# Optimization experiments

Measured on AMD Instinct MI355X. Metric: run time of the kernel, lower is better.

The kernel has to match this reference:

```python
import jax, jax.numpy as jnp
import numpy as np
from jax import lax

N_HEADS = 16
EPS = 1e-6
CHUNK = 128  # chunk size for the causal kv cumsum scan


def causal_dot_product(q, k, v):
    """Equivalent to cumsum over outer-products: out[l] = q[l] . sum_{j<=l} k[j] v[j]^T.
    Chunked lax.scan avoids materializing the [B,H,L,D,M] tensor.
    q,k: [B,H,L,D], v: [B,H,L,M] -> [B,H,L,M]."""
    B, H, L, D = q.shape
    M = v.shape[-1]
    nc = L // CHUNK
    qc = q.reshape(B, H, nc, CHUNK, D).transpose(2, 0, 1, 3, 4)
    kc = k.reshape(B, H, nc, CHUNK, D).transpose(2, 0, 1, 3, 4)
    vc = v.reshape(B, H, nc, CHUNK, M).transpose(2, 0, 1, 3, 4)

    def step(kv_carry, inp):
        qb, kb, vb = inp  # [B,H,C,D], [B,H,C,D], [B,H,C,M]
        kv = jnp.einsum('bhcd,bhcm->bhcdm', kb, vb)
        kv_cum = jnp.cumsum(kv, axis=2) + kv_carry[:, :, None]
        out = jnp.einsum('bhcd,bhcdm->bhcm', qb, kv_cum)
        return kv_cum[:, :, -1], out

    init = jnp.zeros((B, H, D, M), q.dtype)
    _, outs = lax.scan(step, init, (qc, kc, vc))  # outs: [nc,B,H,C,M]
    return outs.transpose(1, 2, 0, 3, 4).reshape(B, H, L, M)


def flow_attention_causal(x, Wq, bq, Wk, bk, Wv, bv, Wo, bo):
    B, L, _ = x.shape
    d_model = Wq.shape[1]
    H = N_HEADS
    # projections -> [B,H,L,D]
    q = (x @ Wq + bq).reshape(B, L, H, -1).transpose(0, 2, 1, 3)
    k = (x @ Wk + bk).reshape(B, L, H, -1).transpose(0, 2, 1, 3)
    v = (x @ Wv + bv).reshape(B, L, H, -1).transpose(0, 2, 1, 3)
    # kernel_method = sigmoid
    q = jax.nn.sigmoid(q)
    k = jax.nn.sigmoid(k)

    sink_incoming = 1.0 / jnp.einsum('bhld,bhld->bhl', q + EPS, jnp.cumsum(k, axis=2) + EPS)
    source_outgoing = 1.0 / jnp.einsum('bhld,bhld->bhl', k + EPS, jnp.cumsum(q, axis=2) + EPS)
    normal = (jnp.arange(L, dtype=x.dtype) + 1.0)[None, None, :]  # [1,1,L]
    sink_incoming = sink_incoming * normal
    source_outgoing = source_outgoing * normal

    conserved_sink = jnp.einsum(
        'bhld,bhld->bhl', q + EPS,
        jnp.cumsum(k * source_outgoing[..., None], axis=2) + EPS) / normal
    conserved_source = jnp.einsum(
        'bhld,bhld->bhl', k + EPS,
        jnp.cumsum(q * sink_incoming[..., None], axis=2) + EPS) / normal

    sink_allocation = jax.nn.sigmoid(conserved_sink)
    cs = jnp.exp(conserved_source)
    source_competition = cs / jnp.cumsum(cs, axis=-1) * normal

    out = causal_dot_product(
        q * (sink_incoming / normal)[..., None],
        k,
        v * source_competition[..., None]) * sink_allocation[..., None]
    out = out.transpose(0, 2, 1, 3).reshape(B, L, d_model)
    return out @ Wo + bo  # dropout is identity at eval


def setup_inputs() -> dict:
    key = jax.random.key(0)
    ks = jax.random.split(key, 9)
    B, L, d_model = 4, 4096, 1024
    s = 0.02
    return {
        'x': jax.random.normal(ks[0], (B, L, d_model), dtype=jnp.float32),
        'Wq': jax.random.normal(ks[1], (d_model, d_model), dtype=jnp.float32) * s,
        'bq': jnp.zeros((d_model,), dtype=jnp.float32),
        'Wk': jax.random.normal(ks[2], (d_model, d_model), dtype=jnp.float32) * s,
        'bk': jnp.zeros((d_model,), dtype=jnp.float32),
        'Wv': jax.random.normal(ks[3], (d_model, d_model), dtype=jnp.float32) * s,
        'bv': jnp.zeros((d_model,), dtype=jnp.float32),
        'Wo': jax.random.normal(ks[4], (d_model, d_model), dtype=jnp.float32) * s,
        'bo': jnp.zeros((d_model,), dtype=jnp.float32),
    }


def reference(x, Wq, bq, Wk, bk, Wv, bv, Wo, bo):
    return flow_attention_causal(x, Wq, bq, Wk, bk, Wv, bv, Wo, bo)
```

## Files before the change

kernel.cpp:

```cpp
#include <hip/hip_runtime.h>
#include <stdint.h>

#define B_ 4
#define L_ 4096
#define DM 1024
#define H_ 16
#define D_ 64
#define BH (B_*H_)
#define N_ (B_*L_)
#define CS 128
#define NC (L_/CS)
#define SC 64
#define NSC (L_/SC)
#define EPSF 1e-6f

typedef unsigned short u16;
typedef unsigned int   u32;
typedef __attribute__((ext_vector_type(8))) short s16x8;
typedef __attribute__((ext_vector_type(4))) float f32x4;

__device__ __forceinline__ float bf2f(u16 u){
  union { u32 i; float f; } v; v.i = ((u32)u) << 16; return v.f;
}
__device__ __forceinline__ u16 f2bf(float f){
  union { float f; u32 i; } v; v.f = f;
  u32 i = v.i;
  return (u16)((i + 0x7fffu + ((i >> 16) & 1u)) >> 16);
}
__device__ __forceinline__ void gload16(const void* g, void* l){
  __builtin_amdgcn_global_load_lds(
      (const __attribute__((address_space(1))) u32*)g,
      (__attribute__((address_space(3))) u32*)l, 16, 0, 0);
}
__device__ __forceinline__ f32x4 mfma16(s16x8 a, s16x8 b, f32x4 c){
  return __builtin_amdgcn_mfma_f32_16x16x32_bf16(a, b, c, 0, 0, 0);
}
__device__ __forceinline__ float sigmoidf_(float x){ return 1.0f/(1.0f+__expf(-x)); }

__global__ void cvt_kernel(const float* __restrict__ in, u16* __restrict__ out, int n4){
  int i = blockIdx.x * blockDim.x + threadIdx.x;
  if (i >= n4) return;
  float4 v = ((const float4*)in)[i];
  union { u16 s[4]; uint2 u; } o;
  o.s[0]=f2bf(v.x); o.s[1]=f2bf(v.y); o.s[2]=f2bf(v.z); o.s[3]=f2bf(v.w);
  ((uint2*)out)[i] = o.u;
}

__global__ __launch_bounds__(256) void transpose_w4_kernel(
    const float* __restrict__ Wq, const float* __restrict__ Wk,
    const float* __restrict__ Wv, const float* __restrict__ Wo,
    u16* __restrict__ wqkvT, u16* __restrict__ woT){
  __shared__ float t[64][65];
  int z = blockIdx.z;
  const float* W = (z==0) ? Wq : (z==1) ? Wk : (z==2) ? Wv : Wo;
  u16* WT = (z<3) ? (wqkvT + (size_t)z*DM*DM) : woT;
  int n0 = blockIdx.x * 64, k0 = blockIdx.y * 64;
  int tx = threadIdx.x & 63, ty = threadIdx.x >> 6;
  #pragma unroll
  for (int s = 0; s < 64; s += 4)
    t[ty + s][tx] = W[(size_t)(k0 + ty + s) * DM + n0 + tx];
  __syncthreads();
  #pragma unroll
  for (int s = 0; s < 64; s += 4)
    WT[(size_t)(n0 + ty + s) * DM + k0 + tx] = f2bf(t[tx][ty + s]);
}

template<int QKV>
__global__ __launch_bounds__(512, 2) void gemm256_kernel(
    const u16* __restrict__ A, const u16* __restrict__ BT,
    const float* __restrict__ biasq, const float* __restrict__ biask, const float* __restrict__ biasv,
    u16* __restrict__ oq, u16* __restrict__ ok, u16* __restrict__ ov,
    float* __restrict__ outf,
    float* __restrict__ sumQ, float* __restrict__ sumK, int NBY)
{
  __shared__ __align__(16) u16 smem[65536];
  char* smb = (char*)smem;
  int tid = threadIdx.x;
  int wave = tid >> 6, lane = tid & 63;
  int wm = wave >> 2, wn = wave & 3;
  int nwg = gridDim.x;
  int q8 = nwg >> 3;
  int id = blockIdx.x;
  int id2 = (id & 7) * q8 + (id >> 3);
  int bx = id2 / NBY, by = id2 % NBY;
  int m0 = bx * 256, n0 = by * 256;
  int srcq = (tid & 7) ^ ((tid >> 3) & 7);
  const u16* aRow = A  + (size_t)(m0 + (tid >> 3)) * 1024 + srcq * 8;
  const u16* bRow = BT + (size_t)(n0 + (tid >> 3)) * 1024 + srcq * 8;

  f32x4 acc[8][4];
  #pragma unroll
  for (int i=0;i<8;i++)
    #pragma unroll
    for (int j=0;j<4;j++) acc[i][j] = (f32x4){0.f,0.f,0.f,0.f};

  int fr = lane & 15, q = lane >> 4;
  int aoff0 = fr*128 + (((q ^ (lane&3)) + 4*((lane>>2)&1)) << 4);
  int aoff1 = fr*128 + (((q ^ (lane&3)) + 4*(1 ^ ((lane>>2)&1))) << 4);

  #define STAGE(s, t) { \
    _Pragma("unroll") \
    for (int i_ = 0; i_ < 4; i_++){ \
      gload16(aRow + (size_t)(t)*64 + (size_t)i_*65536, smb + (s)*32768 + i_*8192 + tid*16); \
      gload16(bRow + (size_t)(t)*64 + (size_t)i_*65536, smb + 65536 + (s)*32768 + i_*8192 + tid*16); \
    } }

  #define COMPUTE(s) { \
    const char* Ab_ = smb + (s)*32768 + wm*16384; \
    const char* Bb_ = smb + 65536 + (s)*32768 + wn*8192; \
    _Pragma("unroll") \
    for (int kk_ = 0; kk_ < 2; kk_++){ \
      int off_ = kk_ ? aoff1 : aoff0; \
      s16x8 af_[8], bf_[4]; \
      _Pragma("unroll") \
      for (int mi_ = 0; mi_ < 8; mi_++) af_[mi_] = *(const s16x8*)(Ab_ + mi_*2048 + off_); \
      _Pragma("unroll") \
      for (int ni_ = 0; ni_ < 4; ni_++) bf_[ni_] = *(const s16x8*)(Bb_ + ni_*2048 + off_); \
      _Pragma("unroll") \
      for (int mi_ = 0; mi_ < 8; mi_++) \
        _Pragma("unroll") \
        for (int ni_ = 0; ni_ < 4; ni_++) \
          acc[mi_][ni_] = mfma16(af_[mi_], bf_[ni_], acc[mi_][ni_]); \
    } }

  STAGE(0, 0)
  STAGE(1, 1)
  for (int t = 0; t < 14; t++){
    asm volatile("s_waitcnt vmcnt(8)" ::: "memory");
    __builtin_amdgcn_s_barrier();
    asm volatile("" ::: "memory");
    COMPUTE(t & 1)
    asm volatile("s_waitcnt lgkmcnt(0)" ::: "memory");
    __builtin_amdgcn_s_barrier();
    asm volatile("" ::: "memory");
    STAGE(t & 1, t + 2)
  }
  asm volatile("s_waitcnt vmcnt(8)" ::: "memory");
  __builtin_amdgcn_s_barrier();
  asm volatile("" ::: "memory");
  COMPUTE(0)
  asm volatile("s_waitcnt vmcnt(0)" ::: "memory");
  __builtin_amdgcn_s_barrier();
  asm volatile("" ::: "memory");
  COMPUTE(1)

  int colblk = n0 + wn*64;
  int which  = QKV ? (colblk >> 10) : 0;
  int cl0    = QKV ? (colblk & 1023) : colblk;
  const float* bias = QKV ? (which==0 ? biasq : (which==1 ? biask : biasv)) : biasq;
  u16* outp = QKV ? (which==0 ? oq : (which==1 ? ok : ov)) : (u16*)0;
  float cs0[4] = {0.f,0.f,0.f,0.f}, cs1[4] = {0.f,0.f,0.f,0.f};
  #pragma unroll
  for (int mi = 0; mi < 8; mi++){
    int row = m0 + wm*128 + mi*16 + (lane>>4)*4;
    #pragma unroll
    for (int ni = 0; ni < 4; ni++){
      int cl = cl0 + ni*16 + fr;
      float bv = bias[cl];
      #pragma unroll
      for (int r = 0; r < 4; r++){
        float val = acc[mi][ni][r] + bv;
        if (QKV){
          if (which < 2) val = sigmoidf_(val);
          outp[(size_t)(row + r) * 1024 + cl] = f2bf(val);
          if (which < 2){ if (mi < 4) cs0[ni] += val; else cs1[ni] += val; }
        } else {
          outf[(size_t)(row + r) * 1024 + cl] = val;
        }
      }
    }
  }
  if (QKV && which < 2){
    float* sums = (which==0) ? sumQ : sumK;
    int bh = (m0 >> 12) * H_ + ((colblk & 1023) >> 6);
    int sc0 = ((m0 & 4095) >> 6) + wm*2;
    #pragma unroll
    for (int h2 = 0; h2 < 2; h2++){
      #pragma unroll
      for (int ni = 0; ni < 4; ni++){
        float s = h2 ? cs1[ni] : cs0[ni];
        s += __shfl_xor(s, 16);
        s += __shfl_xor(s, 32);
        if (lane < 16) sums[((size_t)bh*NSC + sc0 + h2)*64 + ni*16 + fr] = s;
      }
    }
  }
  #undef STAGE
  #undef COMPUTE
}

__global__ __launch_bounds__(64) void scan2_kernel(float* __restrict__ A, float* __restrict__ Bv){
  int bh = blockIdx.x, d = threadIdx.x;
  float ra = 0.f, rb = 0.f;
  for (int g = 0; g < NSC; g += 16){
    float ta[16], tb[16];
    #pragma unroll
    for (int j = 0; j < 16; j++){
      size_t o = ((size_t)bh * NSC + g + j) * 64 + d;
      ta[j] = A[o]; tb[j] = Bv[o];
    }
    #pragma unroll
    for (int j = 0; j < 16; j++){
      size_t o = ((size_t)bh * NSC + g + j) * 64 + d;
      A[o] = ra; Bv[o] = rb;
      ra += ta[j]; rb += tb[j];
    }
  }
}

__global__ __launch_bounds__(64) void siso_fused_kernel(
    const u16* __restrict__ q, const u16* __restrict__ k,
    const float* __restrict__ sumQx, const float* __restrict__ sumKx,
    float* __restrict__ si, float* __restrict__ so,
    float* __restrict__ sumQsi, float* __restrict__ sumKso)
{
  __shared__ u16 cq[64*64];
  __shared__ u16 ck[64*64];
  __shared__ float siv[64], sov[64];
  int bhc = blockIdx.x; int bh = bhc >> 6, sc = bhc & 63;
  int b = bh >> 4, h = bh & 15;
  int lane = threadIdx.x;
  size_t gbase = ((size_t)(b*L_ + sc*SC))*DM + h*D_;
  size_t lb = (size_t)bh*L_ + sc*SC;
  {
    float runQ = sumQx[bhc*64 + lane];
    float runK = sumKx[bhc*64 + lane];
    for (int l = 0; l < SC; l++){
      runQ += bf2f(q[gbase + (size_t)l*DM + lane]);
      runK += bf2f(k[gbase + (size_t)l*DM + lane]);
      int sw = lane ^ (l & 31);
      cq[l*64 + sw] = f2bf(runQ);
      ck[l*64 + sw] = f2bf(runK);
    }
  }
  __syncthreads();
  {
    int l = lane;
    const u16* qrow = q + gbase + (size_t)l*DM;
    const u16* krow = k + gbase + (size_t)l*DM;
    uint4 qr[8], kr[8];
    #pragma unroll
    for (int j=0;j<8;j++){ qr[j]=((const uint4*)qrow)[j]; kr[j]=((const uint4*)krow)[j]; }
    const u16* qp = (const u16*)qr; const u16* kp = (const u16*)kr;
    float a = 0.f, b2 = 0.f;
    #pragma unroll
    for (int d = 0; d < 64; d++){
      int sw = d ^ (l & 31);
      a  += (bf2f(qp[d])+EPSF) * (bf2f(ck[l*64+sw])+EPSF);
      b2 += (bf2f(kp[d])+EPSF) * (bf2f(cq[l*64+sw])+EPSF);
    }
    float n = (float)(sc*SC + l + 1);
    float vsi = n/a, vso = n/b2;
    si[lb+l] = vsi; so[lb+l] = vso;
    siv[l] = vsi;   sov[l] = vso;
    __syncthreads();
    #pragma unroll
    for (int d = 0; d < 64; d++){
      int sw = d ^ (l & 31);
      cq[l*64 + sw] = qp[d];
      ck[l*64 + sw] = kp[d];
    }
  }
  __syncthreads();
  {
    float sq = 0.f, sk = 0.f;
    for (int l = 0; l < SC; l++){
      int sw = lane ^ (l & 31);
      sq += bf2f(cq[l*64 + sw]) * siv[l];
      sk += bf2f(ck[l*64 + sw]) * sov[l];
    }
    sumQsi[bhc*64 + lane] = sq;
    sumKso[bhc*64 + lane] = sk;
  }
}

__global__ __launch_bounds__(64) void cons_fused_kernel(
    const u16* __restrict__ q, const u16* __restrict__ k,
    const float* __restrict__ si, const float* __restrict__ so,
    const float* __restrict__ sumQsiX, const float* __restrict__ sumKsoX,
    float* __restrict__ csrc, float* __restrict__ sall, float* __restrict__ csSum)
{
  __shared__ u16 cq[64*64];
  __shared__ u16 ck[64*64];
  __shared__ float siv[64], sov[64];
  int bhc = blockIdx.x; int bh = bhc >> 6, sc = bhc & 63;
  int b = bh >> 4, h = bh & 15;
  int lane = threadIdx.x;
  size_t gbase = ((size_t)(b*L_ + sc*SC))*DM + h*D_;
  size_t lb = (size_t)bh*L_ + sc*SC;
  siv[lane] = si[lb + lane];
  sov[lane] = so[lb + lane];
  __syncthreads();
  {
    float runQ = sumQsiX[bhc*64 + lane];
    float runK = sumKsoX[bhc*64 + lane];
    for (int l = 0; l < SC; l++){
      runQ += bf2f(q[gbase + (size_t)l*DM + lane]) * siv[l];
      runK += bf2f(k[gbase + (size_t)l*DM + lane]) * sov[l];
      int sw = lane ^ (l & 31);
      cq[l*64 + sw] = f2bf(runQ);
      ck[l*64 + sw] = f2bf(runK);
    }
  }
  __syncthreads();
  {
    int l = lane;
    const u16* qrow = q + gbase + (size_t)l*DM;
    const u16* krow = k + gbase + (size_t)l*DM;
    uint4 qr[8], kr[8];
    #pragma unroll
    for (int j=0;j<8;j++){ qr[j]=((const uint4*)qrow)[j]; kr[j]=((const uint4*)krow)[j]; }
    const u16* qp = (const u16*)qr; const u16* kp = (const u16*)kr;
    float a = 0.f, b2 = 0.f;
    #pragma unroll
    for (int d = 0; d < 64; d++){
      int sw = d ^ (l & 31);
      a  += (bf2f(qp[d])+EPSF) * (bf2f(ck[l*64+sw])+EPSF);
      b2 += (bf2f(kp[d])+EPSF) * (bf2f(cq[l*64+sw])+EPSF);
    }
    float inv = 1.0f / (float)(sc*SC + l + 1);
    sall[lb+l] = sigmoidf_(a * inv);
    float cs = b2 * inv;
    csrc[lb+l] = cs;
    float e = __expf(cs);
    #pragma unroll
    for (int off = 32; off > 0; off >>= 1) e += __shfl_xor(e, off);
    if (lane == 0) csSum[bhc] = e;
  }
}

__global__ __launch_bounds__(64) void scomp_kernel(
    const float* __restrict__ csrc, const float* __restrict__ csSum,
    float* __restrict__ scomp){
  int bhc = blockIdx.x; int bh = bhc >> 6, sc = bhc & 63;
  int lane = threadIdx.x;
  float v2 = (lane < sc) ? csSum[bh*NSC + lane] : 0.f;
  #pragma unroll
  for (int o = 32; o > 0; o >>= 1) v2 += __shfl_xor(v2, o);
  float off = v2;
  size_t idx = (size_t)bh * L_ + sc * SC + lane;
  float cs = __expf(csrc[idx]);
  float run = cs;
  #pragma unroll
  for (int o = 1; o < 64; o <<= 1){
    float t = __shfl_up(run, o);
    if (lane >= o) run += t;
  }
  scomp[idx] = cs / (off + run) * (float)(sc*SC + lane + 1);
}

__global__ __launch_bounds__(256) void vk_chunk_kernel(
    const u16* __restrict__ k, const u16* __restrict__ v,
    const float* __restrict__ scomp, float* __restrict__ vkc){
  __shared__ float ks[32][64];
  __shared__ float vs[32][64];
  int bhc = blockIdx.x; int bh = bhc >> 5, c = bhc & 31;
  int b = bh >> 4, h = bh & 15;
  int tid = threadIdx.x;
  int m = tid >> 2, d0 = (tid & 3) * 16;
  float acc[16];
  #pragma unroll
  for (int j = 0; j < 16; j++) acc[j] = 0.f;
  size_t gbase = ((size_t)(b * L_ + c * CS)) * DM + h * D_;
  size_t sbase = (size_t)bh * L_ + c * CS;
  int r = tid >> 3, cc = (tid & 7) * 8;
  for (int s0 = 0; s0 < CS; s0 += 32){
    __syncthreads();
    float sc = scomp[sbase + s0 + r];
    uint4 ku = *(const uint4*)(k + gbase + (size_t)(s0 + r) * DM + cc);
    uint4 vu = *(const uint4*)(v + gbase + (size_t)(s0 + r) * DM + cc);
    const u16* kp = (const u16*)&ku; const u16* vp = (const u16*)&vu;
    #pragma unroll
    for (int j = 0; j < 8; j++){
      ks[r][cc + j] = bf2f(kp[j]);
      vs[r][cc + j] = bf2f(vp[j]) * sc;
    }
    __syncthreads();
    #pragma unroll
    for (int i = 0; i < 32; i++){
      float vm = vs[i][m];
      #pragma unroll
      for (int j4 = 0; j4 < 4; j4++){
        float4 kk = *(const float4*)&ks[i][d0 + j4*4];
        acc[j4*4+0] += vm * kk.x; acc[j4*4+1] += vm * kk.y;
        acc[j4*4+2] += vm * kk.z; acc[j4*4+3] += vm * kk.w;
      }
    }
  }
  float* outp = vkc + (size_t)bhc * (D_*D_) + m * D_ + d0;
  #pragma unroll
  for (int j = 0; j < 16; j++) outp[j] = acc[j];
}

__global__ __launch_bounds__(256) void vk_scan_kernel(float* __restrict__ vkc){
  int idx = blockIdx.x * 256 + threadIdx.x;
  int bh = idx >> 12;
  int e  = idx & 4095;
  size_t base = ((size_t)bh * NC) * 4096 + e;
  float run = 0.f;
  for (int g = 0; g < NC; g += 16){
    float tv[16];
    #pragma unroll
    for (int j = 0; j < 16; j++) tv[j] = vkc[base + (size_t)(g + j) * 4096];
    #pragma unroll
    for (int j = 0; j < 16; j++){
      vkc[base + (size_t)(g + j) * 4096] = run;
      run += tv[j];
    }
  }
}

__global__ __launch_bounds__(256) void attn_kernel(
    const u16* __restrict__ q, const u16* __restrict__ k, const u16* __restrict__ v,
    const float* __restrict__ si, const float* __restrict__ scomp, const float* __restrict__ salloc,
    const float* __restrict__ vkc, u16* __restrict__ attnout)
{
  __shared__ __align__(16) u16 qs[128*64];
  __shared__ __align__(16) u16 ks2[128*64];
  __shared__ __align__(16) u16 vts[64*128];
  __shared__ __align__(16) u16 vks[64*64];
  __shared__ __align__(16) u16 ss[128*64];
  int bhc = blockIdx.x; int bh = bhc >> 5, c = bhc & 31;
  int b = bh >> 4, h = bh & 15;
  int tid = threadIdx.x, wave = tid >> 6, lane = tid & 63;
  size_t gbase = ((size_t)(b * L_ + c * CS)) * DM + h * D_;
  size_t sbase = (size_t)bh * L_ + c * CS;
  {
    int r = tid >> 1;
    int cc = (tid & 1) * 32;
    int l = c * CS + r;
    float qscale = si[sbase + r] / (float)(l + 1);
    float vscale = scomp[sbase + r];
    #pragma unroll
    for (int j = 0; j < 4; j++){
      uint4 qu = *(const uint4*)(q + gbase + (size_t)r * DM + cc + j*8);
      uint4 kuv = *(const uint4*)(k + gbase + (size_t)r * DM + cc + j*8);
      uint4 vu = *(const uint4*)(v + gbase + (size_t)r * DM + cc + j*8);
      const u16* qp = (const u16*)&qu; const u16* vp = (const u16*)&vu;
      u16 tmp[8];
      #pragma unroll
      for (int e = 0; e < 8; e++) tmp[e] = f2bf(bf2f(qp[e]) * qscale);
      *(uint4*)&qs[r*64 + cc + j*8] = *(uint4*)tmp;
      *(uint4*)&ks2[r*64 + cc + j*8] = kuv;
      #pragma unroll
      for (int e = 0; e < 8; e++) vts[(cc + j*8 + e)*128 + r] = f2bf(bf2f(vp[e]) * vscale);
    }
    const float* vkp = vkc + (size_t)bhc * (D_*D_) + tid * 16;
    u16 tv[16];
    #pragma unroll
    for (int e = 0; e < 16; e++) tv[e] = f2bf(vkp[e]);
    *(uint4*)&vks[tid*16]   = *(uint4*)&tv[0];
    *(uint4*)&vks[tid*16+8] = *(uint4*)&tv[8];
  }
  __syncthreads();
  int t0 = wave, t1 = 7 - wave;
  int fr = lane & 15, kg = (lane >> 4) * 8;
  f32x4 acc[2][4];
  #pragma unroll
  for (int i=0;i<2;i++)
    #pragma unroll
    for (int j=0;j<4;j++) acc[i][j] = (f32x4){0.f,0.f,0.f,0.f};
  s16x8 aq[2][2];
  #pragma unroll
  for (int ti = 0; ti < 2; ti++){
    int t = ti ? t1 : t0;
    #pragma unroll
    for (int kk = 0; kk < 2; kk++)
      aq[ti][kk] = *(const s16x8*)&qs[(t*16 + fr)*64 + kk*32 + kg];
  }
  #pragma unroll
  for (int mt = 0; mt < 4; mt++){
    #pragma unroll
    for (int kk = 0; kk < 2; kk++){
      s16x8 bv = *(const s16x8*)&vks[(mt*16 + fr)*64 + kk*32 + kg];
      acc[0][mt] = mfma16(aq[0][kk], bv, acc[0][mt]);
      acc[1][mt] = mfma16(aq[1][kk], bv, acc[1][mt]);
    }
  }
  for (int jt2 = 0; jt2 < 2; jt2++){
    __syncthreads();
    #pragma unroll
    for (int ti = 0; ti < 2; ti++){
      int t = ti ? t1 : t0;
      #pragma unroll
      for (int u = 0; u < 4; u++){
        int jj = jt2*4 + u;
        f32x4 sacc = (f32x4){0.f,0.f,0.f,0.f};
        if (jj <= t){
          #pragma unroll
          for (int kk = 0; kk < 2; kk++){
            s16x8 bkf = *(const s16x8*)&ks2[(jj*16 + fr)*64 + kk*32 + kg];
            sacc = mfma16(aq[ti][kk], bkf, sacc);
          }
        }
        int lrow = t*16 + (lane>>4)*4;
        int jcol = jj*16 + fr;
        #pragma unroll
        for (int r = 0; r < 4; r++){
          float sv = (jcol <= lrow + r) ? sacc[r] : 0.f;
          ss[(lrow + r)*64 + u*16 + fr] = f2bf(sv);
        }
      }
    }
    __syncthreads();
    #pragma unroll
    for (int ti = 0; ti < 2; ti++){
      int t = ti ? t1 : t0;
      #pragma unroll
      for (int ks = 0; ks < 2; ks++){
        if (jt2*64 + ks*32 <= t*16 + 15){
          s16x8 as = *(const s16x8*)&ss[(t*16 + fr)*64 + ks*32 + kg];
          #pragma unroll
          for (int mt = 0; mt < 4; mt++){
            s16x8 bvv = *(const s16x8*)&vts[(mt*16 + fr)*128 + jt2*64 + ks*32 + kg];
            acc[ti][mt] = mfma16(as, bvv, acc[ti][mt]);
          }
        }
      }
    }
  }
  #pragma unroll
  for (int ti = 0; ti < 2; ti++){
    int t = ti ? t1 : t0;
    int lrow = t*16 + (lane>>4)*4;
    #pragma unroll
    for (int r = 0; r < 4; r++){
      float sa = salloc[sbase + lrow + r];
      size_t orow = ((size_t)(b * L_ + c * CS + lrow + r)) * DM + h * D_;
      #pragma unroll
      for (int mt = 0; mt < 4; mt++){
        attnout[orow + mt*16 + fr] = f2bf(acc[ti][mt][r] * sa);
      }
    }
  }
}

extern "C" void kernel_launch(void* const* d_in, const int* in_sizes, int n_in,
                              void* d_out, int out_size, void* d_ws, size_t ws_size,
                              hipStream_t stream){
  (void)in_sizes; (void)n_in; (void)out_size; (void)ws_size;
  const float* x  = (const float*)d_in[0];
  const float* Wq = (const float*)d_in[1];
  const float* bq = (const float*)d_in[2];
  const float* Wk = (const float*)d_in[3];
  const float* bk = (const float*)d_in[4];
  const float* Wv = (const float*)d_in[5];
  const float* bv = (const float*)d_in[6];
  const float* Wo = (const float*)d_in[7];
  const float* bo = (const float*)d_in[8];

  char* p = (char*)d_ws;
  auto carve = [&](size_t bytes) -> void* {
    void* r = (void*)p; p += (bytes + 255) & ~(size_t)255; return r;
  };
  u16* xb    = (u16*)carve((size_t)N_*DM*2);
  u16* wqkvT = (u16*)carve((size_t)3*DM*DM*2);
  u16* woT   = (u16*)carve((size_t)DM*DM*2);
  u16* qb  = (u16*)carve((size_t)N_*DM*2);
  u16* kb  = (u16*)carve((size_t)N_*DM*2);
  u16* vb  = (u16*)carve((size_t)N_*DM*2);
  u16* ao  = (u16*)carve((size_t)N_*DM*2);
  float* si   = (float*)carve((size_t)BH*L_*4);
  float* so   = (float*)carve((size_t)BH*L_*4);
  float* csrc = (float*)carve((size_t)BH*L_*4);
  float* sall = (float*)carve((size_t)BH*L_*4);
  float* scmp = (float*)carve((size_t)BH*L_*4);
  float* sumQ   = (float*)carve((size_t)BH*NSC*D_*4);
  float* sumK   = (float*)carve((size_t)BH*NSC*D_*4);
  float* sumQsi = (float*)carve((size_t)BH*NSC*D_*4);
  float* sumKso = (float*)carve((size_t)BH*NSC*D_*4);
  float* csSum  = (float*)carve((size_t)BH*NSC*4);
  float* vkc    = (float*)carve((size_t)BH*NC*(size_t)(D_*D_)*4);

  cvt_kernel<<<(N_*DM/4 + 255)/256, 256, 0, stream>>>(x, xb, N_*DM/4);
  transpose_w4_kernel<<<dim3(DM/64, DM/64, 4), 256, 0, stream>>>(Wq, Wk, Wv, Wo, wqkvT, woT);
  gemm256_kernel<1><<<dim3((N_/256)*(3*DM/256)), 512, 0, stream>>>(
      xb, wqkvT, bq, bk, bv, qb, kb, vb, nullptr, sumQ, sumK, 3*DM/256);
  scan2_kernel<<<BH, 64, 0, stream>>>(sumQ, sumK);
  siso_fused_kernel<<<BH*NSC, 64, 0, stream>>>(qb, kb, sumQ, sumK, si, so, sumQsi, sumKso);
  scan2_kernel<<<BH, 64, 0, stream>>>(sumQsi, sumKso);
  cons_fused_kernel<<<BH*NSC, 64, 0, stream>>>(qb, kb, si, so, sumQsi, sumKso, csrc, sall, csSum);
  scomp_kernel<<<BH*NSC, 64, 0, stream>>>(csrc, csSum, scmp);
  vk_chunk_kernel<<<BH*NC, 256, 0, stream>>>(kb, vb, scmp, vkc);
  vk_scan_kernel<<<(BH*D_*D_)/256, 256, 0, stream>>>(vkc);
  attn_kernel<<<BH*NC, 256, 0, stream>>>(qb, kb, vb, si, scmp, sall, vkc, ao);
  gemm256_kernel<0><<<dim3((N_/256)*(DM/256)), 512, 0, stream>>>(
      ao, woT, bo, bo, bo, nullptr, nullptr, nullptr, (float*)d_out, nullptr, nullptr, DM/256);
}
```

Before: 364.6 us.

## Replace 256x256 double-buffered GEMM with simpler 128x128 single-buffered GEMM

Both projection GEMMs move from a 256x256 tile, 512-thread kernel with a two-stage software pipeline of async global-to-LDS loads to a 128x128 tile, 256-thread kernel. The new kernel takes 32-wide K steps through a single LDS buffer with two barriers per step and no overlap of loads with MFMA work. This cuts LDS and register use, which should allow more resident workgroups and more blocks in the grid. In exchange it halves data reuse per tile and loses the load/compute pipelining.

Result: slower. 388.2 us (+6.5%).

```diff
diff --git a/kernel.cpp b/kernel.cpp
--- a/kernel.cpp
+++ b/kernel.cpp
@@ -66,93 +66,69 @@
 }
 
 template<int QKV>
-__global__ __launch_bounds__(512, 2) void gemm256_kernel(
+__global__ __launch_bounds__(256) void gemm128_kernel(
     const u16* __restrict__ A, const u16* __restrict__ BT,
     const float* __restrict__ biasq, const float* __restrict__ biask, const float* __restrict__ biasv,
     u16* __restrict__ oq, u16* __restrict__ ok, u16* __restrict__ ov,
     float* __restrict__ outf,
     float* __restrict__ sumQ, float* __restrict__ sumK, int NBY)
 {
-  __shared__ __align__(16) u16 smem[65536];
-  char* smb = (char*)smem;
+  __shared__ __align__(16) u16 As[128*32];
+  __shared__ __align__(16) u16 Bs[128*32];
   int tid = threadIdx.x;
   int wave = tid >> 6, lane = tid & 63;
-  int wm = wave >> 2, wn = wave & 3;
-  int nwg = gridDim.x;
-  int q8 = nwg >> 3;
-  int id = blockIdx.x;
+  int wr = wave >> 1, wc = wave & 1;
+  int nwg = gridDim.x, q8 = nwg >> 3, id = blockIdx.x;
   int id2 = (id & 7) * q8 + (id >> 3);
   int bx = id2 / NBY, by = id2 % NBY;
-  int m0 = bx * 256, n0 = by * 256;
-  int srcq = (tid & 7) ^ ((tid >> 3) & 7);
-  const u16* aRow = A  + (size_t)(m0 + (tid >> 3)) * 1024 + srcq * 8;
-  const u16* bRow = BT + (size_t)(n0 + (tid >> 3)) * 1024 + srcq * 8;
-
-  f32x4 acc[8][4];
-  #pragma unroll
-  for (int i=0;i<8;i++)
+  int m0 = bx * 128, n0 = by * 128;
+  int r0 = tid >> 2;
+  int srcq = (tid & 3) ^ ((tid >> 3) & 3);
+  const u16* aptr0 = A  + (size_t)(m0 + r0)      * 1024 + srcq * 8;
+  const u16* aptr1 = A  + (size_t)(m0 + 64 + r0) * 1024 + srcq * 8;
+  const u16* bptr0 = BT + (size_t)(n0 + r0)      * 1024 + srcq * 8;
+  const u16* bptr1 = BT + (size_t)(n0 + 64 + r0) * 1024 + srcq * 8;
+  u16* asd0 = &As[tid*8]; u16* asd1 = &As[2048 + tid*8];
+  u16* bsd0 = &Bs[tid*8]; u16* bsd1 = &Bs[2048 + tid*8];
+
+  f32x4 acc[4][4];
+  #pragma unroll
+  for (int i=0;i<4;i++)
     #pragma unroll
     for (int j=0;j<4;j++) acc[i][j] = (f32x4){0.f,0.f,0.f,0.f};
 
   int fr = lane & 15, q = lane >> 4;
-  int aoff0 = fr*128 + (((q ^ (lane&3)) + 4*((lane>>2)&1)) << 4);
-  int aoff1 = fr*128 + (((q ^ (lane&3)) + 4*(1 ^ ((lane>>2)&1))) << 4);
-
-  #define STAGE(s, t) { \
-    _Pragma("unroll") \
-    for (int i_ = 0; i_ < 4; i_++){ \
-      gload16(aRow + (size_t)(t)*64 + (size_t)i_*65536, smb + (s)*32768 + i_*8192 + tid*16); \
-      gload16(bRow + (size_t)(t)*64 + (size_t)i_*65536, smb + 65536 + (s)*32768 + i_*8192 + tid*16); \
-    } }
-
-  #define COMPUTE(s) { \
-    const char* Ab_ = smb + (s)*32768 + wm*16384; \
-    const char* Bb_ = smb + 65536 + (s)*32768 + wn*8192; \
-    _Pragma("unroll") \
-    for (int kk_ = 0; kk_ < 2; kk_++){ \
-      int off_ = kk_ ? aoff1 : aoff0; \
-      s16x8 af_[8], bf_[4]; \
-      _Pragma("unroll") \
-      for (int mi_ = 0; mi_ < 8; mi_++) af_[mi_] = *(const s16x8*)(Ab_ + mi_*2048 + off_); \
-      _Pragma("unroll") \
-      for (int ni_ = 0; ni_ < 4; ni_++) bf_[ni_] = *(const s16x8*)(Bb_ + ni_*2048 + off_); \
-      _Pragma("unroll") \
-      for (int mi_ = 0; mi_ < 8; mi_++) \
-        _Pragma("unroll") \
-        for (int ni_ = 0; ni_ < 4; ni_++) \
-          acc[mi_][ni_] = mfma16(af_[mi_], bf_[ni_], acc[mi_][ni_]); \
-    } }
-
-  STAGE(0, 0)
-  STAGE(1, 1)
-  for (int t = 0; t < 14; t++){
-    asm volatile("s_waitcnt vmcnt(8)" ::: "memory");
-    __builtin_amdgcn_s_barrier();
-    asm volatile("" ::: "memory");
-    COMPUTE(t & 1)
-    asm volatile("s_waitcnt lgkmcnt(0)" ::: "memory");
-    __builtin_amdgcn_s_barrier();
-    asm volatile("" ::: "memory");
-    STAGE(t & 1, t + 2)
-  }
-  asm volatile("s_waitcnt vmcnt(8)" ::: "memory");
-  __builtin_amdgcn_s_barrier();
-  asm volatile("" ::: "memory");
-  COMPUTE(0)
-  asm volatile("s_waitcnt vmcnt(0)" ::: "memory");
-  __builtin_amdgcn_s_barrier();
-  asm volatile("" ::: "memory");
-  COMPUTE(1)
-
-  int colblk = n0 + wn*64;
+  int csw = (q ^ ((fr >> 1) & 3)) << 4;
+  int abase = (wr*64 + fr) * 64 + csw;
+  int bbase = (wc*64 + fr) * 64 + csw;
+
+  for (int kb = 0; kb < 32; kb++){
+    __syncthreads();
+    gload16(aptr0, asd0); gload16(aptr1, asd1);
+    gload16(bptr0, bsd0); gload16(bptr1, bsd1);
+    aptr0 += 32; aptr1 += 32; bptr0 += 32; bptr1 += 32;
+    __syncthreads();
+    s16x8 af[4], bfr[4];
+    #pragma unroll
+    for (int mi=0;mi<4;mi++) af[mi]  = *(const s16x8*)((const char*)As + abase + mi*1024);
+    #pragma unroll
+    for (int ni=0;ni<4;ni++) bfr[ni] = *(const s16x8*)((const char*)Bs + bbase + ni*1024);
+    #pragma unroll
+    for (int mi=0;mi<4;mi++)
+      #pragma unroll
+      for (int ni=0;ni<4;ni++)
+        acc[mi][ni] = mfma16(af[mi], bfr[ni], acc[mi][ni]);
+  }
+
+  int colblk = n0 + wc*64;
   int which  = QKV ? (colblk >> 10) : 0;
   int cl0    = QKV ? (colblk & 1023) : colblk;
   const float* bias = QKV ? (which==0 ? biasq : (which==1 ? biask : biasv)) : biasq;
   u16* outp = QKV ? (which==0 ? oq : (which==1 ? ok : ov)) : (u16*)0;
-  float cs0[4] = {0.f,0.f,0.f,0.f}, cs1[4] = {0.f,0.f,0.f,0.f};
-  #pragma unroll
-  for (int mi = 0; mi < 8; mi++){
-    int row = m0 + wm*128 + mi*16 + (lane>>4)*4;
+  float csum[4] = {0.f,0.f,0.f,0.f};
+  #pragma unroll
+  for (int mi = 0; mi < 4; mi++){
+    int row = m0 + wr*64 + mi*16 + (lane>>4)*4;
     #pragma unroll
     for (int ni = 0; ni < 4; ni++){
       int cl = cl0 + ni*16 + fr;
@@ -163,7 +139,7 @@
         if (QKV){
           if (which < 2) val = sigmoidf_(val);
           outp[(size_t)(row + r) * 1024 + cl] = f2bf(val);
-          if (which < 2){ if (mi < 4) cs0[ni] += val; else cs1[ni] += val; }
+          if (which < 2) csum[ni] += val;
         } else {
           outf[(size_t)(row + r) * 1024 + cl] = val;
         }
@@ -173,20 +149,15 @@
   if (QKV && which < 2){
     float* sums = (which==0) ? sumQ : sumK;
     int bh = (m0 >> 12) * H_ + ((colblk & 1023) >> 6);
-    int sc0 = ((m0 & 4095) >> 6) + wm*2;
-    #pragma unroll
-    for (int h2 = 0; h2 < 2; h2++){
-      #pragma unroll
-      for (int ni = 0; ni < 4; ni++){
-        float s = h2 ? cs1[ni] : cs0[ni];
-        s += __shfl_xor(s, 16);
-        s += __shfl_xor(s, 32);
-        if (lane < 16) sums[((size_t)bh*NSC + sc0 + h2)*64 + ni*16 + fr] = s;
-      }
-    }
-  }
-  #undef STAGE
-  #undef COMPUTE
+    int sc = ((m0 & 4095) >> 6) + wr;
+    #pragma unroll
+    for (int ni = 0; ni < 4; ni++){
+      float s = csum[ni];
+      s += __shfl_xor(s, 16);
+      s += __shfl_xor(s, 32);
+      if (lane < 16) sums[((size_t)bh*NSC + sc)*64 + ni*16 + fr] = s;
+    }
+  }
 }
 
 __global__ __launch_bounds__(64) void scan2_kernel(float* __restrict__ A, float* __restrict__ Bv){
@@ -574,8 +545,8 @@
 
   cvt_kernel<<<(N_*DM/4 + 255)/256, 256, 0, stream>>>(x, xb, N_*DM/4);
   transpose_w4_kernel<<<dim3(DM/64, DM/64, 4), 256, 0, stream>>>(Wq, Wk, Wv, Wo, wqkvT, woT);
-  gemm256_kernel<1><<<dim3((N_/256)*(3*DM/256)), 512, 0, stream>>>(
-      xb, wqkvT, bq, bk, bv, qb, kb, vb, nullptr, sumQ, sumK, 3*DM/256);
+  gemm128_kernel<1><<<dim3((N_/128)*(3*DM/128)), 256, 0, stream>>>(
+      xb, wqkvT, bq, bk, bv, qb, kb, vb, nullptr, sumQ, sumK, 3*DM/128);
   scan2_kernel<<<BH, 64, 0, stream>>>(sumQ, sumK);
   siso_fused_kernel<<<BH*NSC, 64, 0, stream>>>(qb, kb, sumQ, sumK, si, so, sumQsi, sumKso);
   scan2_kernel<<<BH, 64, 0, stream>>>(sumQsi, sumKso);
@@ -584,6 +555,6 @@
   vk_chunk_kernel<<<BH*NC, 256, 0, stream>>>(kb, vb, scmp, vkc);
   vk_scan_kernel<<<(BH*D_*D_)/256, 256, 0, stream>>>(vkc);
   attn_kernel<<<BH*NC, 256, 0, stream>>>(qb, kb, vb, si, scmp, sall, vkc, ao);
-  gemm256_kernel<0><<<dim3((N_/256)*(DM/256)), 512, 0, stream>>>(
-      ao, woT, bo, bo, bo, nullptr, nullptr, nullptr, (float*)d_out, nullptr, nullptr, DM/256);
-}
+  gemm128_kernel<0><<<dim3((N_/128)*(DM/128)), 256, 0, stream>>>(
+      ao, woT, bo, bo, bo, nullptr, nullptr, nullptr, (float*)d_out, nullptr, nullptr, DM/128);
+}
```

## Use MFMA with swizzled bf16 LDS tiles for per-chunk V^T K outer-product sums

Applied to the files above, without the earlier changes.

The per-chunk V^T·K accumulation moves from a scalar fp32 FMA loop over shared memory to bf16 MFMA instructions. The k and scaled-v chunks are staged transposed in LDS with an XOR swizzle to avoid bank conflicts. The scan kernel now writes the exclusive prefix as bf16 into a separate buffer, so the attention kernel loads bf16 directly instead of converting fp32. This cuts ALU work and memory traffic, but rounds scaled v to bf16 before the outer-product sum, which may reduce accuracy.

New measurement: 337.6 us. 1.08x faster.

```diff
diff --git a/kernel.cpp b/kernel.cpp
--- a/kernel.cpp
+++ b/kernel.cpp
@@ -352,47 +352,57 @@
 __global__ __launch_bounds__(256) void vk_chunk_kernel(
     const u16* __restrict__ k, const u16* __restrict__ v,
     const float* __restrict__ scomp, float* __restrict__ vkc){
-  __shared__ float ks[32][64];
-  __shared__ float vs[32][64];
+  __shared__ __align__(16) u16 vt[64*128];
+  __shared__ __align__(16) u16 kt[64*128];
   int bhc = blockIdx.x; int bh = bhc >> 5, c = bhc & 31;
   int b = bh >> 4, h = bh & 15;
-  int tid = threadIdx.x;
-  int m = tid >> 2, d0 = (tid & 3) * 16;
-  float acc[16];
-  #pragma unroll
-  for (int j = 0; j < 16; j++) acc[j] = 0.f;
+  int tid = threadIdx.x, wave = tid >> 6, lane = tid & 63;
   size_t gbase = ((size_t)(b * L_ + c * CS)) * DM + h * D_;
   size_t sbase = (size_t)bh * L_ + c * CS;
-  int r = tid >> 3, cc = (tid & 7) * 8;
-  for (int s0 = 0; s0 < CS; s0 += 32){
-    __syncthreads();
-    float sc = scomp[sbase + s0 + r];
-    uint4 ku = *(const uint4*)(k + gbase + (size_t)(s0 + r) * DM + cc);
-    uint4 vu = *(const uint4*)(v + gbase + (size_t)(s0 + r) * DM + cc);
-    const u16* kp = (const u16*)&ku; const u16* vp = (const u16*)&vu;
-    #pragma unroll
-    for (int j = 0; j < 8; j++){
-      ks[r][cc + j] = bf2f(kp[j]);
-      vs[r][cc + j] = bf2f(vp[j]) * sc;
-    }
-    __syncthreads();
-    #pragma unroll
-    for (int i = 0; i < 32; i++){
-      float vm = vs[i][m];
-      #pragma unroll
-      for (int j4 = 0; j4 < 4; j4++){
-        float4 kk = *(const float4*)&ks[i][d0 + j4*4];
-        acc[j4*4+0] += vm * kk.x; acc[j4*4+1] += vm * kk.y;
-        acc[j4*4+2] += vm * kk.z; acc[j4*4+3] += vm * kk.w;
+  {
+    int r = tid >> 1;
+    int cc = (tid & 1) * 32;
+    float vscale = scomp[sbase + r];
+    #pragma unroll
+    for (int j = 0; j < 4; j++){
+      uint4 ku = *(const uint4*)(k + gbase + (size_t)r * DM + cc + j*8);
+      uint4 vu = *(const uint4*)(v + gbase + (size_t)r * DM + cc + j*8);
+      const u16* kp = (const u16*)&ku; const u16* vp = (const u16*)&vu;
+      #pragma unroll
+      for (int e = 0; e < 8; e++){
+        int m = cc + j*8 + e;
+        int idx = m*128 + ((((r >> 3) ^ (m & 7)) << 3) | (r & 7));
+        vt[idx] = f2bf(bf2f(vp[e]) * vscale);
+        kt[idx] = kp[e];
       }
     }
   }
-  float* outp = vkc + (size_t)bhc * (D_*D_) + m * D_ + d0;
-  #pragma unroll
-  for (int j = 0; j < 16; j++) outp[j] = acc[j];
-}
-
-__global__ __launch_bounds__(256) void vk_scan_kernel(float* __restrict__ vkc){
+  __syncthreads();
+  int fr = lane & 15, q = lane >> 4;
+  int mt = wave;
+  f32x4 acc[4];
+  #pragma unroll
+  for (int i = 0; i < 4; i++) acc[i] = (f32x4){0.f,0.f,0.f,0.f};
+  #pragma unroll
+  for (int ks = 0; ks < 4; ks++){
+    int lc = ks*4 + q;
+    int off = ((lc ^ (fr & 7)) << 3);
+    s16x8 av = *(const s16x8*)&vt[(mt*16 + fr)*128 + off];
+    #pragma unroll
+    for (int nt = 0; nt < 4; nt++){
+      s16x8 bk = *(const s16x8*)&kt[(nt*16 + fr)*128 + off];
+      acc[nt] = mfma16(av, bk, acc[nt]);
+    }
+  }
+  float* outp = vkc + (size_t)bhc * (D_*D_);
+  #pragma unroll
+  for (int nt = 0; nt < 4; nt++)
+    #pragma unroll
+    for (int r = 0; r < 4; r++)
+      outp[(mt*16 + q*4 + r)*64 + nt*16 + fr] = acc[nt][r];
+}
+
+__global__ __launch_bounds__(256) void vk_scan_kernel(const float* __restrict__ vkc, u16* __restrict__ vkb){
   int idx = blockIdx.x * 256 + threadIdx.x;
   int bh = idx >> 12;
   int e  = idx & 4095;
@@ -404,7 +414,7 @@
     for (int j = 0; j < 16; j++) tv[j] = vkc[base + (size_t)(g + j) * 4096];
     #pragma unroll
     for (int j = 0; j < 16; j++){
-      vkc[base + (size_t)(g + j) * 4096] = run;
+      vkb[base + (size_t)(g + j) * 4096] = f2bf(run);
       run += tv[j];
     }
   }
@@ -413,7 +423,7 @@
 __global__ __launch_bounds__(256) void attn_kernel(
     const u16* __restrict__ q, const u16* __restrict__ k, const u16* __restrict__ v,
     const float* __restrict__ si, const float* __restrict__ scomp, const float* __restrict__ salloc,
-    const float* __restrict__ vkc, u16* __restrict__ attnout)
+    const u16* __restrict__ vkb, u16* __restrict__ attnout)
 {
   __shared__ __align__(16) u16 qs[128*64];
   __shared__ __align__(16) u16 ks2[128*64];
@@ -445,12 +455,9 @@
       #pragma unroll
       for (int e = 0; e < 8; e++) vts[(cc + j*8 + e)*128 + r] = f2bf(bf2f(vp[e]) * vscale);
     }
-    const float* vkp = vkc + (size_t)bhc * (D_*D_) + tid * 16;
-    u16 tv[16];
-    #pragma unroll
-    for (int e = 0; e < 16; e++) tv[e] = f2bf(vkp[e]);
-    *(uint4*)&vks[tid*16]   = *(uint4*)&tv[0];
-    *(uint4*)&vks[tid*16+8] = *(uint4*)&tv[8];
+    const u16* vkp = vkb + (size_t)bhc * (D_*D_) + tid * 16;
+    *(uint4*)&vks[tid*16]   = *(const uint4*)(vkp);
+    *(uint4*)&vks[tid*16+8] = *(const uint4*)(vkp + 8);
   }
   __syncthreads();
   int t0 = wave, t1 = 7 - wave;
@@ -571,6 +578,7 @@
   float* sumKso = (float*)carve((size_t)BH*NSC*D_*4);
   float* csSum  = (float*)carve((size_t)BH*NSC*4);
   float* vkc    = (float*)carve((size_t)BH*NC*(size_t)(D_*D_)*4);
+  u16*   vkb    = (u16*)carve((size_t)BH*NC*(size_t)(D_*D_)*2);
 
   cvt_kernel<<<(N_*DM/4 + 255)/256, 256, 0, stream>>>(x, xb, N_*DM/4);
   transpose_w4_kernel<<<dim3(DM/64, DM/64, 4), 256, 0, stream>>>(Wq, Wk, Wv, Wo, wqkvT, woT);
@@ -582,8 +590,8 @@
   cons_fused_kernel<<<BH*NSC, 64, 0, stream>>>(qb, kb, si, so, sumQsi, sumKso, csrc, sall, csSum);
   scomp_kernel<<<BH*NSC, 64, 0, stream>>>(csrc, csSum, scmp);
   vk_chunk_kernel<<<BH*NC, 256, 0, stream>>>(kb, vb, scmp, vkc);
-  vk_scan_kernel<<<(BH*D_*D_)/256, 256, 0, stream>>>(vkc);
-  attn_kernel<<<BH*NC, 256, 0, stream>>>(qb, kb, vb, si, scmp, sall, vkc, ao);
+  vk_scan_kernel<<<(BH*D_*D_)/256, 256, 0, stream>>>(vkc, vkb);
+  attn_kernel<<<BH*NC, 256, 0, stream>>>(qb, kb, vb, si, scmp, sall, vkb, ao);
   gemm256_kernel<0><<<dim3((N_/256)*(DM/256)), 512, 0, stream>>>(
       ao, woT, bo, bo, bo, nullptr, nullptr, nullptr, (float*)d_out, nullptr, nullptr, DM/256);
 }
```
